# Kernel optimization log

Measured on AMD Instinct MI355X. Metric: run time of the kernel, lower is better.

The kernel has to match this reference:

```python
import jax, jax.numpy as jnp
import numpy as np

B, S, H, V = 64, 256, 1024, 10000


def setup_inputs() -> dict:
    key = jax.random.key(0)
    ks = jax.random.split(key, 16)
    s = 1.0 / np.sqrt(H)
    return {
        "input_seq": jax.random.randint(ks[0], (B,), 0, V),
        "last_hidden": jax.random.normal(ks[1], (1, 1, H), jnp.float32),
        "encoder_outputs": jax.random.normal(ks[2], (S, B, H), jnp.float32),
        "emb_table": jax.random.normal(ks[3], (V, H), jnp.float32) * s,
        "W_ih": jax.random.normal(ks[4], (3 * H, H), jnp.float32) * s,
        "W_hh": jax.random.normal(ks[5], (3 * H, H), jnp.float32) * s,
        "b_ih": jax.random.normal(ks[6], (3 * H,), jnp.float32) * s,
        "b_hh": jax.random.normal(ks[7], (3 * H,), jnp.float32) * s,
        "W_attn": jax.random.normal(ks[8], (H, 2 * H), jnp.float32) * s,
        "b_attn": jax.random.normal(ks[9], (H,), jnp.float32) * s,
        "v_attn": jax.random.normal(ks[10], (H,), jnp.float32) * s,
        "W_concat": jax.random.normal(ks[11], (H, 2 * H), jnp.float32) * s,
        "b_concat": jax.random.normal(ks[12], (H,), jnp.float32) * s,
        "W_out": jax.random.normal(ks[13], (V, H), jnp.float32) * s,
        "b_out": jax.random.normal(ks[14], (V,), jnp.float32) * s,
    }


def _gru_scan(x_seq, h0, W_ih, W_hh, b_ih, b_hh):
    # x_seq: [T, H] (here T == batch dim, per the module's batch_first quirk)
    def step(h, x):
        gi = x @ W_ih.T + b_ih   # [3H]
        gh = h @ W_hh.T + b_hh   # [3H]
        ir, iz, inn = jnp.split(gi, 3)
        hr, hz, hn = jnp.split(gh, 3)
        r = jax.nn.sigmoid(ir + hr)
        z = jax.nn.sigmoid(iz + hz)
        n = jnp.tanh(inn + r * hn)
        h_new = (1.0 - z) * n + z * h
        return h_new, h_new

    h_last, outs = jax.lax.scan(step, h0, x_seq)
    return outs, h_last


def reference(input_seq, last_hidden, encoder_outputs, emb_table, W_ih, W_hh,
              b_ih, b_hh, W_attn, b_attn, v_attn, W_concat, b_concat, W_out, b_out):
    embedded = emb_table[input_seq]                       # [B, H]
    # GRU fed [1, B, H] with batch_first=True -> recurs over B with one hidden
    rnn_output, h_last = _gru_scan(embedded, last_hidden[0, 0], W_ih, W_hh, b_ih, b_hh)
    hidden = h_last[None, None, :]                        # [1, 1, H]

    # concat attention: score(b,i) = v . (W_attn @ [h_b ; enc_ib] + b_attn)
    enc = jnp.transpose(encoder_outputs, (1, 0, 2))       # [B, S, H]
    h_bc = jnp.broadcast_to(rnn_output[:, None, :], (B, S, H))
    cat = jnp.concatenate([h_bc, enc], axis=-1)           # [B, S, 2H]
    energy = jnp.einsum('bsk,hk->bsh', cat, W_attn) + b_attn
    scores = jnp.einsum('bsh,h->bs', energy, v_attn)      # [B, S]
    attn_weights = jax.nn.softmax(scores, axis=-1)[:, None, :]  # [B, 1, S]

    context = jnp.einsum('bs,bsh->bh', attn_weights[:, 0, :], enc)  # [B, H]
    concat_input = jnp.concatenate([rnn_output, context], axis=-1)  # [B, 2H]
    concat_output = jnp.tanh(concat_input @ W_concat.T + b_concat)  # [B, H]
    output = concat_output @ W_out.T + b_out                        # [B, V]
    return output, hidden, attn_weights
```

## Files before the change

### kernel.cpp

```cpp
#include <hip/hip_runtime.h>
#include <math.h>

#define kH  1024
#define kB  64
#define kS  256
#define kV  10000
#define kH3 3072

typedef unsigned long long u64;

__device__ __forceinline__ float warp_sum(float v) {
#pragma unroll
  for (int off = 32; off > 0; off >>= 1) v += __shfl_down(v, off, 64);
  return v;
}
__device__ __forceinline__ float warp_max_all(float v) {
#pragma unroll
  for (int off = 32; off > 0; off >>= 1) v = fmaxf(v, __shfl_xor(v, off, 64));
  return v;
}
__device__ __forceinline__ float warp_sum_all(float v) {
#pragma unroll
  for (int off = 32; off > 0; off >>= 1) v += __shfl_xor(v, off, 64);
  return v;
}
__device__ __forceinline__ float sigmoidf_(float x) {
  return __fdividef(1.0f, 1.0f + __expf(-x));
}
__device__ __forceinline__ float tanhf_(float x) {
  const float t = __expf(-2.0f * fabsf(x));
  const float r = __fdividef(1.0f - t, 1.0f + t);
  return copysignf(r, x);
}

__global__ __launch_bounds__(256) void k_pre(const int* __restrict__ seq,
    const float* __restrict__ emb, const float* __restrict__ W_ih,
    const float* __restrict__ b_ih, const float* __restrict__ W_attn,
    const float* __restrict__ v_attn, float* __restrict__ GI,
    float* __restrict__ w2h) {
  __shared__ float xl[64 * 65];
  __shared__ float wl[16 * 64];
  __shared__ float4 red[256];
  const int tid = threadIdx.x;

  if (blockIdx.x < 192) {
    const int rblk = blockIdx.x * 16;
    const int t = tid & 63;
    const int g = tid >> 6;
    float acc[4] = {0.f, 0.f, 0.f, 0.f};

    for (int c = 0; c < 16; ++c) {
      const int h0 = c * 64;
      {
        const int tx = tid >> 2;
        const int tok = seq[tx];
        const float* xr = emb + (size_t)tok * kH + h0;
#pragma unroll
        for (int k = 0; k < 4; ++k) {
          const int slot = (tid & 3) + 4 * k;
          const float4 v = *(const float4*)(xr + slot * 4);
          const int hh = slot * 4;
          xl[(hh + 0) * 65 + tx] = v.x;
          xl[(hh + 1) * 65 + tx] = v.y;
          xl[(hh + 2) * 65 + tx] = v.z;
          xl[(hh + 3) * 65 + tx] = v.w;
        }
      }
      {
        const int r = tid >> 4, c4 = tid & 15;
        *(float4*)&wl[r * 64 + c4 * 4] =
            ((const float4*)(W_ih + (size_t)(rblk + r) * kH + h0))[c4];
      }
      __syncthreads();
#pragma unroll
      for (int q = 0; q < 16; ++q) {
        const int hh = q * 4;
        const float x0 = xl[(hh + 0) * 65 + t];
        const float x1 = xl[(hh + 1) * 65 + t];
        const float x2 = xl[(hh + 2) * 65 + t];
        const float x3 = xl[(hh + 3) * 65 + t];
#pragma unroll
        for (int i = 0; i < 4; ++i) {
          const float4 wq = *(const float4*)&wl[(g * 4 + i) * 64 + hh];
          acc[i] += wq.x * x0 + wq.y * x1 + wq.z * x2 + wq.w * x3;
        }
      }
      __syncthreads();
    }
    const float4 bi = *(const float4*)(b_ih + rblk + g * 4);
    float4 o;
    o.x = acc[0] + bi.x; o.y = acc[1] + bi.y;
    o.z = acc[2] + bi.z; o.w = acc[3] + bi.w;
    *(float4*)(GI + (size_t)t * kH3 + rblk + g * 4) = o;

  } else {
    const int wb = blockIdx.x - 192;
    const int k0 = kH + wb * 4;
    float ax = 0, ay = 0, az = 0, aw = 0;
    for (int h = tid; h < kH; h += 256) {
      const float vh = v_attn[h];
      const float4 wq = *(const float4*)(W_attn + (size_t)h * 2048 + k0);
      ax += vh * wq.x; ay += vh * wq.y; az += vh * wq.z; aw += vh * wq.w;
    }
    red[tid] = make_float4(ax, ay, az, aw);
    __syncthreads();
    for (int s = 128; s > 0; s >>= 1) {
      if (tid < s) {
        const float4 a = red[tid], b = red[tid + s];
        red[tid] = make_float4(a.x + b.x, a.y + b.y, a.z + b.z, a.w + b.w);
      }
      __syncthreads();
    }
    if (tid == 0) *(float4*)(w2h + wb * 4) = red[0];
  }
}

__global__ __launch_bounds__(256) void k_gru(const float* __restrict__ h0,
    const float* __restrict__ W_hh, const float* __restrict__ b_hh,
    const float* __restrict__ GI, float* __restrict__ rnn,
    u64* __restrict__ step) {
  __shared__ float4 wlds4[12 * 256];
  __shared__ __align__(16) float hs[2][kH];
  const int tid  = threadIdx.x;
  const int lane = tid & 63;
  const int w    = tid >> 6;
  const int bid  = blockIdx.x;
  const int j    = bid * 4 + w;

#pragma unroll
  for (int c = 0; c < 12; ++c) {
    const int f    = c * 256 + tid;
    const int row  = f >> 8;
    const int col4 = f & 255;
    const int q    = row >> 2, r = row & 3;
    wlds4[f] = ((const float4*)(W_hh + ((size_t)q * kH + bid * 4 + r) * kH))[col4];
  }

  const float bhr = b_hh[j];
  const float bhz = b_hh[kH + j];
  const float bhn = b_hh[2 * kH + j];

  for (int t = 0; t < kB; ++t) {
    float gir = GI[(size_t)t * kH3 + j];
    float giz = GI[(size_t)t * kH3 + kH + j];
    float gin = GI[(size_t)t * kH3 + 2 * kH + j];
    asm volatile("" :: "v"(gir), "v"(giz), "v"(gin));

    float* hb = hs[t & 1];
    if (t == 0) {
      ((float4*)hb)[tid] = ((const float4*)h0)[tid];
    } else {
      const u64* sb = step + (size_t)(t - 1) * kH;
      const unsigned want = (unsigned)t;
      const int i0 = tid * 4;
      bool done[4] = {false, false, false, false};
      float v[4];
      while (true) {
        bool all = true;
#pragma unroll
        for (int k = 0; k < 4; ++k) {
          if (!done[k]) {
            const u64 x = __hip_atomic_load(&sb[i0 + k],
                __ATOMIC_RELAXED, __HIP_MEMORY_SCOPE_AGENT);
            if ((unsigned)(x >> 32) == want) {
              v[k] = __uint_as_float((unsigned)x);
              done[k] = true;
            } else {
              all = false;
            }
          }
        }
        if (all) break;
        __builtin_amdgcn_s_sleep(1);
      }
#pragma unroll
      for (int k = 0; k < 4; ++k) hb[i0 + k] = v[k];
    }
    __syncthreads();

    float4 hx4[4];
#pragma unroll
    for (int c = 0; c < 4; ++c) hx4[c] = ((const float4*)hb)[lane + 64 * c];

    float d[3];
#pragma unroll
    for (int q = 0; q < 3; ++q) {
      float acc = 0.f;
#pragma unroll
      for (int c = 0; c < 4; ++c) {
        const float4 wq = wlds4[(q * 4 + w) * 256 + lane + 64 * c];
        const float4 h4 = hx4[c];
        acc += wq.x * h4.x + wq.y * h4.y + wq.z * h4.z + wq.w * h4.w;
      }
      d[q] = acc;
    }
#pragma unroll
    for (int q = 0; q < 3; ++q) d[q] = warp_sum(d[q]);

    if (lane == 0) {
      const float ho = hb[j];
      const float r = sigmoidf_(gir + d[0] + bhr);
      const float z = sigmoidf_(giz + d[1] + bhz);
      const float n = tanhf_(gin + r * (d[2] + bhn));
      const float hn = (1.f - z) * n + z * ho;
      rnn[(size_t)t * kH + j] = hn;
      __hip_atomic_store(&step[(size_t)t * kH + j],
                         (((u64)(t + 1)) << 32) | __float_as_uint(hn),
                         __ATOMIC_RELAXED, __HIP_MEMORY_SCOPE_AGENT);
    }
  }
}

__global__ __launch_bounds__(1024) void k_att(const float* __restrict__ enc,
    const float* __restrict__ w2h, const float* __restrict__ rnn,
    float* __restrict__ attn, float* __restrict__ ctx,
    float* __restrict__ hid) {
  __shared__ float scl[kS];
  __shared__ float sm[4], ss[4];
  __shared__ float4 part4[1024];
  const int b = blockIdx.x, tid = threadIdx.x;
  const int lane = tid & 63, w = tid >> 6;

  {
    const float4* wp = (const float4*)w2h + lane * 4;
    const float4 wq0 = wp[0], wq1 = wp[1], wq2 = wp[2], wq3 = wp[3];
    for (int k = 0; k < 16; ++k) {
      const int s = w * 16 + k;
      const float4* ep =
          (const float4*)(enc + ((size_t)s * kB + b) * kH) + lane * 4;
      const float4 e0 = ep[0], e1 = ep[1], e2 = ep[2], e3 = ep[3];
      float acc = e0.x*wq0.x + e0.y*wq0.y + e0.z*wq0.z + e0.w*wq0.w;
      acc += e1.x*wq1.x + e1.y*wq1.y + e1.z*wq1.z + e1.w*wq1.w;
      acc += e2.x*wq2.x + e2.y*wq2.y + e2.z*wq2.z + e2.w*wq2.w;
      acc += e3.x*wq3.x + e3.y*wq3.y + e3.z*wq3.z + e3.w*wq3.w;
      acc = warp_sum(acc);
      if (lane == 0) scl[s] = acc;
    }
  }
  __syncthreads();

  float x = 0.f, e = 0.f;
  if (tid < kS) {
    x = scl[tid];
    const float m = warp_max_all(x);
    if (lane == 0) sm[w] = m;
  }
  __syncthreads();
  if (tid < kS) {
    const float m = fmaxf(fmaxf(sm[0], sm[1]), fmaxf(sm[2], sm[3]));
    e = __expf(x - m);
    const float s = warp_sum_all(e);
    if (lane == 0) ss[w] = s;
  }
  __syncthreads();
  if (tid < kS) {
    const float s = ss[0] + ss[1] + ss[2] + ss[3];
    const float a = e / s;
    attn[b * kS + tid] = a;
    scl[tid] = a;
  }
  if (b < 4 && tid < kS) {
    hid[b * kS + tid] = rnn[63 * kH + b * kS + tid];
  }
  __syncthreads();

  const int hc = tid & 255;
  const int sq = tid >> 8;
  const float4* encb = (const float4*)enc;
  float4 acc = make_float4(0.f, 0.f, 0.f, 0.f);
  const int s0 = sq * 64;
#pragma unroll 4
  for (int s = s0; s < s0 + 64; ++s) {
    const float a = scl[s];
    const float4 v = encb[((size_t)s * kB + b) * 256 + hc];
    acc.x += a * v.x; acc.y += a * v.y; acc.z += a * v.z; acc.w += a * v.w;
  }
  part4[tid] = acc;
  __syncthreads();
  if (tid < 256) {
    const float4 p0 = part4[tid], p1 = part4[tid + 256];
    const float4 p2 = part4[tid + 512], p3 = part4[tid + 768];
    float4 r;
    r.x = p0.x + p1.x + p2.x + p3.x;
    r.y = p0.y + p1.y + p2.y + p3.y;
    r.z = p0.z + p1.z + p2.z + p3.z;
    r.w = p0.w + p1.w + p2.w + p3.w;
    ((float4*)(ctx + (size_t)b * kH))[tid] = r;
  }
}

__global__ __launch_bounds__(256) void k_concat(const float* __restrict__ rnn,
    const float* __restrict__ ctx, const float* __restrict__ W_c,
    const float* __restrict__ b_c, float* __restrict__ coT) {
  const int lane = threadIdx.x & 63;
  const int iq = blockIdx.x >> 2;
  const int bq = blockIdx.x & 3;
  const int i  = iq * 4 + (threadIdx.x >> 6);
  float wreg[32];
  {
    const float4* wp = (const float4*)(W_c + (size_t)i * 2048) + lane * 8;
#pragma unroll
    for (int c = 0; c < 8; ++c) {
      const float4 f = wp[c];
      wreg[c * 4 + 0] = f.x; wreg[c * 4 + 1] = f.y;
      wreg[c * 4 + 2] = f.z; wreg[c * 4 + 3] = f.w;
    }
  }
  const float bc = b_c[i];
  const int jcol = lane * 32;
  const float* xbase = (jcol < kH) ? (rnn + jcol) : (ctx + (jcol - kH));
  for (int b = bq * 16; b < bq * 16 + 16; ++b) {
    const float* xr = xbase + (size_t)b * kH;
    float acc = 0.f;
#pragma unroll
    for (int c = 0; c < 8; ++c) {
      const float4 x = *(const float4*)(xr + c * 4);
      acc += wreg[c * 4 + 0] * x.x + wreg[c * 4 + 1] * x.y +
             wreg[c * 4 + 2] * x.z + wreg[c * 4 + 3] * x.w;
    }
    acc = warp_sum(acc);
    if (lane == 0) coT[(size_t)i * kB + b] = tanhf(acc + bc);
  }
}

__global__ __launch_bounds__(256) void k_out(const float* __restrict__ coT,
    const float* __restrict__ W_out, const float* __restrict__ b_out,
    float* __restrict__ out) {
  __shared__ float wlds[16 * kH];
  const int v0 = blockIdx.x * 16;
  {
    const float4* src = (const float4*)(W_out + (size_t)v0 * kH);
    float4 tmp[16];
#pragma unroll
    for (int c = 0; c < 16; ++c) tmp[c] = src[threadIdx.x + 256 * c];
    float4* dst = (float4*)wlds;
#pragma unroll
    for (int c = 0; c < 16; ++c) dst[threadIdx.x + 256 * c] = tmp[c];
  }
  __syncthreads();

  const int lane = threadIdx.x & 63;
  const int w    = threadIdx.x >> 6;
  float acc[4] = {0.f, 0.f, 0.f, 0.f};
#pragma unroll 2
  for (int h = 0; h < kH; h += 4) {
    const float x0 = coT[(size_t)(h + 0) * kB + lane];
    const float x1 = coT[(size_t)(h + 1) * kB + lane];
    const float x2 = coT[(size_t)(h + 2) * kB + lane];
    const float x3 = coT[(size_t)(h + 3) * kB + lane];
#pragma unroll
    for (int vi = 0; vi < 4; ++vi) {
      const float4 wq = *(const float4*)&wlds[(w * 4 + vi) * kH + h];
      acc[vi] += wq.x * x0 + wq.y * x1 + wq.z * x2 + wq.w * x3;
    }
  }
  const float4 bq = *(const float4*)(b_out + v0 + w * 4);
  float4 r;
  r.x = acc[0] + bq.x; r.y = acc[1] + bq.y;
  r.z = acc[2] + bq.z; r.w = acc[3] + bq.w;
  *(float4*)&out[(size_t)lane * kV + v0 + w * 4] = r;
}

extern "C" void kernel_launch(void* const* d_in, const int* in_sizes, int n_in,
                              void* d_out, int out_size, void* d_ws,
                              size_t ws_size, hipStream_t stream) {
  const int*   seq    = (const int*)  d_in[0];
  const float* h0     = (const float*)d_in[1];
  const float* enc    = (const float*)d_in[2];
  const float* emb    = (const float*)d_in[3];
  const float* W_ih   = (const float*)d_in[4];
  const float* W_hh   = (const float*)d_in[5];
  const float* b_ih   = (const float*)d_in[6];
  const float* b_hh   = (const float*)d_in[7];
  const float* W_attn = (const float*)d_in[8];
  const float* v_attn = (const float*)d_in[10];
  const float* W_conc = (const float*)d_in[11];
  const float* b_conc = (const float*)d_in[12];
  const float* W_outp = (const float*)d_in[13];
  const float* b_outp = (const float*)d_in[14];

  float* out      = (float*)d_out;
  float* out_hid  = out + 640000;
  float* out_attn = out + 641024;

  float* ws = (float*)d_ws;
  float* GI   = ws;
  float* RNN  = ws + 196608;
  u64*   STEP = (u64*)(ws + 262144);
  float* W2H  = ws + 393216;
  float* CTX  = ws + 394240;
  float* COT  = ws + 459776;

  k_pre<<<448, 256, 0, stream>>>(seq, emb, W_ih, b_ih, W_attn, v_attn,
                                 GI, W2H);
  k_gru<<<256, 256, 0, stream>>>(h0, W_hh, b_hh, GI, RNN, STEP);
  k_att<<<64, 1024, 0, stream>>>(enc, W2H, RNN, out_attn, CTX, out_hid);
  k_concat<<<1024, 256, 0, stream>>>(RNN, CTX, W_conc, b_conc, COT);
  k_out<<<625, 256, 0, stream>>>(COT, W_outp, b_outp, out);
}
```

Measured before the change: 542.2 us.

## Split attention into score, softmax, context kernels; transpose rnn/ctx for concat

The single 64-block attention kernel is replaced by separate score, softmax, partial-context and reduction kernels, so the encoder traffic is spread across 256 blocks instead of 64. The GRU now writes its output transposed, and the context is also stored transposed, so the concat GEMV reads activations coalesced per batch lane, with each row split across two wave halves. This adds four kernel launches and extra global round trips for scores and partial contexts, in exchange for more parallelism on the memory-bound encoder reads.

```diff
diff --git a/kernel.cpp b/kernel.cpp
--- a/kernel.cpp
+++ b/kernel.cpp
@@ -117,7 +117,7 @@
 
 __global__ __launch_bounds__(256) void k_gru(const float* __restrict__ h0,
     const float* __restrict__ W_hh, const float* __restrict__ b_hh,
-    const float* __restrict__ GI, float* __restrict__ rnn,
+    const float* __restrict__ GI, float* __restrict__ rnnT,
     u64* __restrict__ step) {
   __shared__ float4 wlds4[12 * 256];
   __shared__ __align__(16) float hs[2][kH];
@@ -203,123 +203,131 @@
       const float z = sigmoidf_(giz + d[1] + bhz);
       const float n = tanhf_(gin + r * (d[2] + bhn));
       const float hn = (1.f - z) * n + z * ho;
-      rnn[(size_t)t * kH + j] = hn;
       __hip_atomic_store(&step[(size_t)t * kH + j],
                          (((u64)(t + 1)) << 32) | __float_as_uint(hn),
                          __ATOMIC_RELAXED, __HIP_MEMORY_SCOPE_AGENT);
-    }
-  }
-}
-
-__global__ __launch_bounds__(1024) void k_att(const float* __restrict__ enc,
-    const float* __restrict__ w2h, const float* __restrict__ rnn,
-    float* __restrict__ attn, float* __restrict__ ctx,
-    float* __restrict__ hid) {
-  __shared__ float scl[kS];
-  __shared__ float sm[4], ss[4];
-  __shared__ float4 part4[1024];
-  const int b = blockIdx.x, tid = threadIdx.x;
+      rnnT[(size_t)j * kB + t] = hn;
+    }
+  }
+}
+
+__global__ __launch_bounds__(256) void k_sc(const float* __restrict__ enc,
+    const float* __restrict__ w2h, float* __restrict__ sc) {
+  const int tid = threadIdx.x;
   const int lane = tid & 63, w = tid >> 6;
-
-  {
-    const float4* wp = (const float4*)w2h + lane * 4;
-    const float4 wq0 = wp[0], wq1 = wp[1], wq2 = wp[2], wq3 = wp[3];
-    for (int k = 0; k < 16; ++k) {
-      const int s = w * 16 + k;
+  const int b = blockIdx.x & 63, q = blockIdx.x >> 6;
+  const float4* wp = (const float4*)w2h + lane * 4;
+  const float4 wq0 = wp[0], wq1 = wp[1], wq2 = wp[2], wq3 = wp[3];
+  const int s0 = q * 64 + w * 16;
+#pragma unroll
+  for (int kb = 0; kb < 4; ++kb) {
+    float acc[4];
+#pragma unroll
+    for (int i = 0; i < 4; ++i) {
+      const int s = s0 + kb * 4 + i;
       const float4* ep =
           (const float4*)(enc + ((size_t)s * kB + b) * kH) + lane * 4;
       const float4 e0 = ep[0], e1 = ep[1], e2 = ep[2], e3 = ep[3];
-      float acc = e0.x*wq0.x + e0.y*wq0.y + e0.z*wq0.z + e0.w*wq0.w;
-      acc += e1.x*wq1.x + e1.y*wq1.y + e1.z*wq1.z + e1.w*wq1.w;
-      acc += e2.x*wq2.x + e2.y*wq2.y + e2.z*wq2.z + e2.w*wq2.w;
-      acc += e3.x*wq3.x + e3.y*wq3.y + e3.z*wq3.z + e3.w*wq3.w;
-      acc = warp_sum(acc);
-      if (lane == 0) scl[s] = acc;
-    }
-  }
+      float a = e0.x*wq0.x + e0.y*wq0.y + e0.z*wq0.z + e0.w*wq0.w;
+      a += e1.x*wq1.x + e1.y*wq1.y + e1.z*wq1.z + e1.w*wq1.w;
+      a += e2.x*wq2.x + e2.y*wq2.y + e2.z*wq2.z + e2.w*wq2.w;
+      a += e3.x*wq3.x + e3.y*wq3.y + e3.z*wq3.z + e3.w*wq3.w;
+      acc[i] = a;
+    }
+#pragma unroll
+    for (int i = 0; i < 4; ++i) acc[i] = warp_sum(acc[i]);
+    if (lane == 0) {
+#pragma unroll
+      for (int i = 0; i < 4; ++i) sc[b * kS + s0 + kb * 4 + i] = acc[i];
+    }
+  }
+}
+
+__global__ __launch_bounds__(256) void k_sm(const float* __restrict__ sc,
+    const float* __restrict__ rnnT, float* __restrict__ attn,
+    float* __restrict__ hid) {
+  __shared__ float sm[4], ss[4];
+  const int b = blockIdx.x, t = threadIdx.x, lane = t & 63, w = t >> 6;
+  const float x = sc[b * kS + t];
+  float m = warp_max_all(x);
+  if (lane == 0) sm[w] = m;
   __syncthreads();
-
-  float x = 0.f, e = 0.f;
-  if (tid < kS) {
-    x = scl[tid];
-    const float m = warp_max_all(x);
-    if (lane == 0) sm[w] = m;
-  }
+  m = fmaxf(fmaxf(sm[0], sm[1]), fmaxf(sm[2], sm[3]));
+  const float e = __expf(x - m);
+  float s = warp_sum_all(e);
+  if (lane == 0) ss[w] = s;
   __syncthreads();
-  if (tid < kS) {
-    const float m = fmaxf(fmaxf(sm[0], sm[1]), fmaxf(sm[2], sm[3]));
-    e = __expf(x - m);
-    const float s = warp_sum_all(e);
-    if (lane == 0) ss[w] = s;
-  }
-  __syncthreads();
-  if (tid < kS) {
-    const float s = ss[0] + ss[1] + ss[2] + ss[3];
-    const float a = e / s;
-    attn[b * kS + tid] = a;
-    scl[tid] = a;
-  }
-  if (b < 4 && tid < kS) {
-    hid[b * kS + tid] = rnn[63 * kH + b * kS + tid];
-  }
-  __syncthreads();
-
-  const int hc = tid & 255;
-  const int sq = tid >> 8;
-  const float4* encb = (const float4*)enc;
-  float4 acc = make_float4(0.f, 0.f, 0.f, 0.f);
-  const int s0 = sq * 64;
+  s = ss[0] + ss[1] + ss[2] + ss[3];
+  attn[b * kS + t] = e / s;
+  if (b < 4) {
+    hid[b * kS + t] = rnnT[(size_t)(b * kS + t) * kB + 63];
+  }
+}
+
+__global__ __launch_bounds__(256) void k_ctx(const float* __restrict__ enc,
+    const float* __restrict__ attn, float* __restrict__ partT) {
+  const int b  = blockIdx.x & 63;
+  const int ch = blockIdx.x >> 6;
+  const int h0 = threadIdx.x * 4;
+  float ax = 0, ay = 0, az = 0, aw = 0;
+  const int s0 = ch * 64;
 #pragma unroll 4
   for (int s = s0; s < s0 + 64; ++s) {
-    const float a = scl[s];
-    const float4 v = encb[((size_t)s * kB + b) * 256 + hc];
-    acc.x += a * v.x; acc.y += a * v.y; acc.z += a * v.z; acc.w += a * v.w;
-  }
-  part4[tid] = acc;
+    const float a = attn[b * kS + s];
+    const float4 v = *(const float4*)(enc + ((size_t)s * kB + b) * kH + h0);
+    ax += a * v.x; ay += a * v.y; az += a * v.z; aw += a * v.w;
+  }
+  float* base = partT + (size_t)ch * (kH * kB);
+  base[(h0 + 0) * kB + b] = ax;
+  base[(h0 + 1) * kB + b] = ay;
+  base[(h0 + 2) * kB + b] = az;
+  base[(h0 + 3) * kB + b] = aw;
+}
+
+__global__ __launch_bounds__(256) void k_ctxsum(const float* __restrict__ partT,
+    float* __restrict__ ctxT) {
+  const int e = blockIdx.x * 256 + threadIdx.x;
+  const float p0 = partT[e];
+  const float p1 = partT[65536 + e];
+  const float p2 = partT[131072 + e];
+  const float p3 = partT[196608 + e];
+  ctxT[e] = p0 + p1 + p2 + p3;
+}
+
+__global__ __launch_bounds__(512) void k_concat(const float* __restrict__ rnnT,
+    const float* __restrict__ ctxT, const float* __restrict__ W_c,
+    const float* __restrict__ b_c, float* __restrict__ coT) {
+  __shared__ float sred[8 * 64];
+  const int tid = threadIdx.x;
+  const int lane = tid & 63;
+  const int g = tid >> 6;
+  const int half = g & 1;
+  const int i = __builtin_amdgcn_readfirstlane(blockIdx.x * 4 + (g >> 1));
+  const float* wr = W_c + (size_t)i * 2048;
+  const int hb = half * 512;
+
+  float a0 = 0.f, a1 = 0.f, a2 = 0.f, a3 = 0.f;
+#pragma unroll 4
+  for (int h = hb; h < hb + 512; h += 4) {
+    const float4 wq = *(const float4*)(wr + h);
+    a0 += wq.x * rnnT[(size_t)(h + 0) * kB + lane];
+    a1 += wq.y * rnnT[(size_t)(h + 1) * kB + lane];
+    a2 += wq.z * rnnT[(size_t)(h + 2) * kB + lane];
+    a3 += wq.w * rnnT[(size_t)(h + 3) * kB + lane];
+  }
+#pragma unroll 4
+  for (int h = hb; h < hb + 512; h += 4) {
+    const float4 wq = *(const float4*)(wr + kH + h);
+    a0 += wq.x * ctxT[(size_t)(h + 0) * kB + lane];
+    a1 += wq.y * ctxT[(size_t)(h + 1) * kB + lane];
+    a2 += wq.z * ctxT[(size_t)(h + 2) * kB + lane];
+    a3 += wq.w * ctxT[(size_t)(h + 3) * kB + lane];
+  }
+  sred[g * 64 + lane] = ((a0 + a1) + (a2 + a3));
   __syncthreads();
-  if (tid < 256) {
-    const float4 p0 = part4[tid], p1 = part4[tid + 256];
-    const float4 p2 = part4[tid + 512], p3 = part4[tid + 768];
-    float4 r;
-    r.x = p0.x + p1.x + p2.x + p3.x;
-    r.y = p0.y + p1.y + p2.y + p3.y;
-    r.z = p0.z + p1.z + p2.z + p3.z;
-    r.w = p0.w + p1.w + p2.w + p3.w;
-    ((float4*)(ctx + (size_t)b * kH))[tid] = r;
-  }
-}
-
-__global__ __launch_bounds__(256) void k_concat(const float* __restrict__ rnn,
-    const float* __restrict__ ctx, const float* __restrict__ W_c,
-    const float* __restrict__ b_c, float* __restrict__ coT) {
-  const int lane = threadIdx.x & 63;
-  const int iq = blockIdx.x >> 2;
-  const int bq = blockIdx.x & 3;
-  const int i  = iq * 4 + (threadIdx.x >> 6);
-  float wreg[32];
-  {
-    const float4* wp = (const float4*)(W_c + (size_t)i * 2048) + lane * 8;
-#pragma unroll
-    for (int c = 0; c < 8; ++c) {
-      const float4 f = wp[c];
-      wreg[c * 4 + 0] = f.x; wreg[c * 4 + 1] = f.y;
-      wreg[c * 4 + 2] = f.z; wreg[c * 4 + 3] = f.w;
-    }
-  }
-  const float bc = b_c[i];
-  const int jcol = lane * 32;
-  const float* xbase = (jcol < kH) ? (rnn + jcol) : (ctx + (jcol - kH));
-  for (int b = bq * 16; b < bq * 16 + 16; ++b) {
-    const float* xr = xbase + (size_t)b * kH;
-    float acc = 0.f;
-#pragma unroll
-    for (int c = 0; c < 8; ++c) {
-      const float4 x = *(const float4*)(xr + c * 4);
-      acc += wreg[c * 4 + 0] * x.x + wreg[c * 4 + 1] * x.y +
-             wreg[c * 4 + 2] * x.z + wreg[c * 4 + 3] * x.w;
-    }
-    acc = warp_sum(acc);
-    if (lane == 0) coT[(size_t)i * kB + b] = tanhf(acc + bc);
+  if (half == 0) {
+    const float tot = sred[g * 64 + lane] + sred[(g + 1) * 64 + lane];
+    coT[(size_t)i * kB + lane] = tanhf(tot + b_c[i]);
   }
 }
 
@@ -384,17 +392,22 @@
   float* out_attn = out + 641024;
 
   float* ws = (float*)d_ws;
-  float* GI   = ws;
-  float* RNN  = ws + 196608;
-  u64*   STEP = (u64*)(ws + 262144);
-  float* W2H  = ws + 393216;
-  float* CTX  = ws + 394240;
-  float* COT  = ws + 459776;
+  float* GI    = ws;
+  float* RNNT  = ws + 196608;
+  u64*   STEP  = (u64*)(ws + 262144);
+  float* W2H   = ws + 393216;
+  float* SC    = ws + 394240;
+  float* PARTT = ws + 410624;
+  float* CTXT  = ws + 672768;
+  float* COT   = ws + 738304;
 
   k_pre<<<448, 256, 0, stream>>>(seq, emb, W_ih, b_ih, W_attn, v_attn,
                                  GI, W2H);
-  k_gru<<<256, 256, 0, stream>>>(h0, W_hh, b_hh, GI, RNN, STEP);
-  k_att<<<64, 1024, 0, stream>>>(enc, W2H, RNN, out_attn, CTX, out_hid);
-  k_concat<<<1024, 256, 0, stream>>>(RNN, CTX, W_conc, b_conc, COT);
+  k_gru<<<256, 256, 0, stream>>>(h0, W_hh, b_hh, GI, RNNT, STEP);
+  k_sc<<<256, 256, 0, stream>>>(enc, W2H, SC);
+  k_sm<<<64, 256, 0, stream>>>(SC, RNNT, out_attn, out_hid);
+  k_ctx<<<256, 256, 0, stream>>>(enc, out_attn, PARTT);
+  k_ctxsum<<<256, 256, 0, stream>>>(PARTT, CTXT);
+  k_concat<<<256, 512, 0, stream>>>(RNNT, CTXT, W_conc, b_conc, COT);
   k_out<<<625, 256, 0, stream>>>(COT, W_outp, b_outp, out);
 }
```

Result: no change. 541.7 us (-0.1%).
